# Kernel optimization log

Measured on AMD Instinct MI355X. Metric: run time of the kernel, lower is better.

Reference implementation:

```python
import jax, jax.numpy as jnp
import numpy as np


def rotary_pos_emb(x):
    # x: [b, h, l, k]; interleaved rotary embedding (pairs are (0,1),(2,3),...)
    dim = x.shape[-1]
    seq = x.shape[-2]
    ts = jnp.arange(0, dim, 2, dtype=jnp.float32)
    inv_freqs = 10000.0 ** (-ts / dim)                      # [dim/2]
    grid = jnp.arange(seq, dtype=jnp.float32)[:, None] * inv_freqs[None, :]  # [l, dim/2]
    sin_embs = jnp.repeat(jnp.sin(grid), 2, axis=-1)[None]  # [1, l, dim] (interleaved repeat)
    cos_embs = jnp.repeat(jnp.cos(grid), 2, axis=-1)[None]
    x1, x2 = x[..., ::2], x[..., 1::2]
    xs = jnp.stack([-x2, x1], axis=-1).reshape(x.shape)     # interleave (-x2, x1)
    return x * cos_embs + xs * sin_embs


def setup_inputs() -> dict:
    key = jax.random.key(0)
    ks = jax.random.split(key, 5)
    b, l, d = 2, 2048, 1024
    scale = 1.0 / np.sqrt(d)
    return {
        "x": jax.random.normal(ks[0], (b, l, d), dtype=jnp.float32),
        "Wq": jax.random.normal(ks[1], (d, d), dtype=jnp.float32) * scale,
        "Wk": jax.random.normal(ks[2], (d, d), dtype=jnp.float32) * scale,
        "Wv": jax.random.normal(ks[3], (d, d), dtype=jnp.float32) * scale,
        "Wo": jax.random.normal(ks[4], (d, d), dtype=jnp.float32) * scale,
        "is_training": 0,
    }


def reference(x, Wq, Wk, Wv, Wo, is_training):
    n_heads = 16
    b, l, d = x.shape
    k_size = d // n_heads
    # NOTE: module scales q by 1/sqrt(model_size), not 1/sqrt(key_size)
    q = (x @ Wq) / jnp.sqrt(jnp.float32(d))
    q = q.reshape(b, l, n_heads, k_size).transpose(0, 2, 1, 3)  # b h l k
    k = (x @ Wk).reshape(b, l, n_heads, k_size).transpose(0, 2, 1, 3)
    v = (x @ Wv).reshape(b, l, n_heads, k_size).transpose(0, 2, 1, 3)
    q = rotary_pos_emb(q)
    k = rotary_pos_emb(k)
    logits = jnp.einsum('bhik,bhjk->bhij', q, k)  # no mask, no dropout (eval)
    a = jax.nn.softmax(logits, axis=-1)
    y = jnp.einsum('bhij,bhjv->bhiv', a, v)
    y = y.transpose(0, 2, 1, 3).reshape(b, l, d)  # b l (h v)
    return y @ Wo
```

## Files before the change

### kernel.cpp

```cpp
#include <hip/hip_runtime.h>
#include <stdint.h>

typedef unsigned short u16;
using short8 = __attribute__((ext_vector_type(8))) short;
using f32x4  = __attribute__((ext_vector_type(4))) float;

typedef __attribute__((address_space(1))) unsigned int gu32;
typedef __attribute__((address_space(3))) unsigned int lu32;

__device__ __forceinline__ void gl2lds16(const u16* g, u16* lds_wave_base) {
    __builtin_amdgcn_global_load_lds(
        (gu32*)(uintptr_t)(const void*)g,
        (lu32*)(uint32_t)(uintptr_t)(void*)lds_wave_base,
        16, 0, 0);
}

__device__ inline float bf2f(u16 u) {
    union { unsigned int i; float f; } v;
    v.i = ((unsigned int)u) << 16;
    return v.f;
}
__device__ inline u16 f2bf(float f) {
    union { float f; unsigned int i; } v;
    v.f = f;
    unsigned int x = v.i;
    return (u16)((x + 0x7fffu + ((x >> 16) & 1u)) >> 16);
}
__device__ inline u16 f2bf_trunc(float f) {
    union { float f; unsigned int i; } v;
    v.f = f;
    return (u16)(v.i >> 16);
}

__global__ __launch_bounds__(256) void cvt_x(const float* __restrict__ x,
                                             u16* __restrict__ xb)
{
    int i = (blockIdx.x * 256 + threadIdx.x) * 4;
    float4 v = *(const float4*)(x + i);
    ushort4 o;
    o.x = f2bf(v.x); o.y = f2bf(v.y); o.z = f2bf(v.z); o.w = f2bf(v.w);
    *(ushort4*)(xb + i) = o;
}

__global__ __launch_bounds__(256) void transpose4_cvt(
    const float* __restrict__ w0, const float* __restrict__ w1,
    const float* __restrict__ w2, const float* __restrict__ w3,
    u16* __restrict__ t0, u16* __restrict__ t1,
    u16* __restrict__ t2, u16* __restrict__ t3)
{
    __shared__ u16 tile[32][33];
    const float* src; u16* dst;
    switch (blockIdx.z) {
        case 0:  src = w0; dst = t0; break;
        case 1:  src = w1; dst = t1; break;
        case 2:  src = w2; dst = t2; break;
        default: src = w3; dst = t3; break;
    }
    int tx = threadIdx.x, ty = threadIdx.y;
    int c0 = blockIdx.x * 32, r0 = blockIdx.y * 32;
    #pragma unroll
    for (int i = 0; i < 4; i++)
        tile[ty + i * 8][tx] = f2bf(src[(size_t)(r0 + ty + i * 8) * 1024 + c0 + tx]);
    __syncthreads();
    #pragma unroll
    for (int i = 0; i < 4; i++)
        dst[(size_t)(c0 + ty + i * 8) * 1024 + r0 + tx] = tile[tx][ty + i * 8];
}

__global__ __launch_bounds__(256) void transpose_v(const u16* __restrict__ Vb,
                                                   u16* __restrict__ VT)
{
    __shared__ u16 t[32][33];
    int bh = blockIdx.z, b = bh >> 4, h = bh & 15;
    int p0 = blockIdx.x * 32, c0 = blockIdx.y * 32;
    int tx = threadIdx.x, ty = threadIdx.y;
    #pragma unroll
    for (int i = 0; i < 4; i++)
        t[ty + i * 8][tx] = Vb[(size_t)(b * 2048 + p0 + ty + i * 8) * 1024 + h * 64 + c0 + tx];
    __syncthreads();
    #pragma unroll
    for (int i = 0; i < 4; i++)
        VT[((size_t)bh * 64 + c0 + ty + i * 8) * 2048 + p0 + tx] = t[tx][ty + i * 8];
}

__global__ __launch_bounds__(256) void gemm_qkv(
    const u16* __restrict__ A, const u16* __restrict__ Bt,
    u16* __restrict__ Qb, u16* __restrict__ Kb, u16* __restrict__ Vb)
{
    __shared__ __align__(16) u16 As[128 * 32];
    __shared__ __align__(16) u16 Bs[128 * 32];

    const int tid  = threadIdx.x;
    const int lane = tid & 63;
    const int wid  = tid >> 6;
    const int quad = lane >> 4;
    const int l15  = lane & 15;
    const int wm   = wid >> 1, wn = wid & 1;

    const int m0 = blockIdx.y * 128;
    const int n0 = blockIdx.x * 128;
    const int mat = n0 >> 10;
    const int ln0 = n0 & 1023;
    u16* C = (mat == 0) ? Qb : (mat == 1 ? Kb : Vb);
    const float scale = (mat == 0) ? 0.03125f : 1.0f;

    f32x4 acc[4][4] = {};

    for (int k0 = 0; k0 < 1024; k0 += 32) {
        #pragma unroll
        for (int it = 0; it < 2; it++) {
            int c   = it * 256 + tid;
            int row = c >> 2;
            int col = ((c & 3) ^ (row & 3)) * 8;
            u16* lbA = &As[(size_t)(it * 256 + wid * 64) * 8];
            u16* lbB = &Bs[(size_t)(it * 256 + wid * 64) * 8];
            gl2lds16(&A [(size_t)(m0 + row) * 1024 + k0 + col], lbA);
            gl2lds16(&Bt[(size_t)(n0 + row) * 1024 + k0 + col], lbB);
        }
        __syncthreads();

        short8 a[4], b[4];
        #pragma unroll
        for (int i = 0; i < 4; i++) {
            int ra = wm * 64 + i * 16 + l15;
            int rb = wn * 64 + i * 16 + l15;
            a[i] = *(const short8*)(&As[ra * 32 + ((quad ^ (ra & 3)) * 8)]);
            b[i] = *(const short8*)(&Bs[rb * 32 + ((quad ^ (rb & 3)) * 8)]);
        }
        #pragma unroll
        for (int i = 0; i < 4; i++)
            #pragma unroll
            for (int j = 0; j < 4; j++)
                acc[i][j] = __builtin_amdgcn_mfma_f32_16x16x32_bf16(a[i], b[j], acc[i][j], 0, 0, 0);
        __syncthreads();
    }

    #pragma unroll
    for (int i = 0; i < 4; i++)
        #pragma unroll
        for (int j = 0; j < 4; j++)
            #pragma unroll
            for (int r = 0; r < 4; r++) {
                int row = m0 + wm * 64 + i * 16 + quad * 4 + r;
                int col = ln0 + wn * 64 + j * 16 + l15;
                C[(size_t)row * 1024 + col] = f2bf(acc[i][j][r] * scale);
            }
}

__global__ __launch_bounds__(256) void gemm_out(
    const u16* __restrict__ A, const u16* __restrict__ Bt, float* __restrict__ C)
{
    __shared__ __align__(16) u16 As[128 * 32];
    __shared__ __align__(16) u16 Bs[128 * 32];

    const int tid  = threadIdx.x;
    const int lane = tid & 63;
    const int wid  = tid >> 6;
    const int quad = lane >> 4;
    const int l15  = lane & 15;
    const int wm   = wid >> 1, wn = wid & 1;

    const int m0 = blockIdx.y * 128;
    const int n0 = blockIdx.x * 128;

    f32x4 acc[4][4] = {};

    for (int k0 = 0; k0 < 1024; k0 += 32) {
        #pragma unroll
        for (int it = 0; it < 2; it++) {
            int c   = it * 256 + tid;
            int row = c >> 2;
            int col = ((c & 3) ^ (row & 3)) * 8;
            u16* lbA = &As[(size_t)(it * 256 + wid * 64) * 8];
            u16* lbB = &Bs[(size_t)(it * 256 + wid * 64) * 8];
            gl2lds16(&A [(size_t)(m0 + row) * 1024 + k0 + col], lbA);
            gl2lds16(&Bt[(size_t)(n0 + row) * 1024 + k0 + col], lbB);
        }
        __syncthreads();

        short8 a[4], b[4];
        #pragma unroll
        for (int i = 0; i < 4; i++) {
            int ra = wm * 64 + i * 16 + l15;
            int rb = wn * 64 + i * 16 + l15;
            a[i] = *(const short8*)(&As[ra * 32 + ((quad ^ (ra & 3)) * 8)]);
            b[i] = *(const short8*)(&Bs[rb * 32 + ((quad ^ (rb & 3)) * 8)]);
        }
        #pragma unroll
        for (int i = 0; i < 4; i++)
            #pragma unroll
            for (int j = 0; j < 4; j++)
                acc[i][j] = __builtin_amdgcn_mfma_f32_16x16x32_bf16(a[i], b[j], acc[i][j], 0, 0, 0);
        __syncthreads();
    }

    #pragma unroll
    for (int i = 0; i < 4; i++)
        #pragma unroll
        for (int j = 0; j < 4; j++)
            #pragma unroll
            for (int r = 0; r < 4; r++) {
                int row = m0 + wm * 64 + i * 16 + quad * 4 + r;
                int col = n0 + wn * 64 + j * 16 + l15;
                C[(size_t)row * 1024 + col] = acc[i][j][r];
            }
}

__global__ __launch_bounds__(256) void rope_k(u16* __restrict__ Q, u16* __restrict__ Kb)
{
    u16* buf = (blockIdx.y == 0) ? Q : Kb;
    int idx = blockIdx.x * 256 + threadIdx.x;
    int row = idx >> 9;
    int p   = idx & 511;
    int pos = row & 2047;
    int i   = p & 31;

    const float ln10000_over_32 = 0.2878231366f;
    float inv = __expf(-(float)i * ln10000_over_32);
    float ang = (float)pos * inv;
    float s, c;
    __sincosf(ang, &s, &c);

    size_t base = (size_t)row * 1024 + (size_t)p * 2;
    float x0 = bf2f(buf[base]);
    float x1 = bf2f(buf[base + 1]);
    buf[base]     = f2bf(x0 * c - x1 * s);
    buf[base + 1] = f2bf(x1 * c + x0 * s);
}

__global__ __launch_bounds__(256) void attn(
    const u16* __restrict__ Q, const u16* __restrict__ Kb,
    const u16* __restrict__ VT, u16* __restrict__ Y)
{
    __shared__ __align__(16) u16 Ks [64 * 64];
    __shared__ __align__(16) u16 VTs[64 * 64];
    __shared__ __align__(16) u16 Ps [4][16 * 72];

    const int tid  = threadIdx.x;
    const int lane = tid & 63, wid = tid >> 6;
    const int quad = lane >> 4, l15 = lane & 15;

    const int bh = blockIdx.x;
    const int qt = blockIdx.y;
    const int bb = bh >> 4, h = bh & 15;

    const size_t base = ((size_t)bb * 2048) * 1024 + (size_t)h * 64;

    short8 qf[2];
    {
        size_t qrow = (size_t)qt * 64 + wid * 16 + l15;
        const u16* qp = Q + base + qrow * 1024;
        qf[0] = *(const short8*)(qp + quad * 8);
        qf[1] = *(const short8*)(qp + 32 + quad * 8);
    }

    f32x4 o[4] = {};
    float l_r[4] = {0.f, 0.f, 0.f, 0.f};

    for (int j0 = 0; j0 < 2048; j0 += 64) {
        __syncthreads();
        #pragma unroll
        for (int it = 0; it < 2; it++) {
            int c   = it * 256 + tid;
            int r   = c >> 3;
            int col = ((c & 7) ^ (r & 7)) * 8;
            u16* lbK = &Ks [(size_t)(it * 256 + wid * 64) * 8];
            u16* lbV = &VTs[(size_t)(it * 256 + wid * 64) * 8];
            gl2lds16(&Kb[base + (size_t)(j0 + r) * 1024 + col], lbK);
            gl2lds16(&VT[((size_t)bh * 64 + r) * 2048 + j0 + col], lbV);
        }
        __syncthreads();

        f32x4 s[4];
        #pragma unroll
        for (int nt = 0; nt < 4; nt++) {
            int R = nt * 16 + l15;
            short8 k0 = *(const short8*)(&Ks[R * 64 + (( quad      ^ (R & 7)) * 8)]);
            short8 k1 = *(const short8*)(&Ks[R * 64 + (((quad + 4) ^ (R & 7)) * 8)]);
            f32x4 z = {};
            z = __builtin_amdgcn_mfma_f32_16x16x32_bf16(qf[0], k0, z, 0, 0, 0);
            z = __builtin_amdgcn_mfma_f32_16x16x32_bf16(qf[1], k1, z, 0, 0, 0);
            s[nt] = z;
        }

        #pragma unroll
        for (int nt = 0; nt < 4; nt++)
            #pragma unroll
            for (int r = 0; r < 4; r++) {
                float p = __expf(s[nt][r]);
                l_r[r] += p;
                Ps[wid][(quad * 4 + r) * 72 + nt * 16 + l15] = f2bf_trunc(p);
            }

        asm volatile("s_waitcnt lgkmcnt(0)" ::: "memory");

        short8 pa0 = *(const short8*)(&Ps[wid][l15 * 72 + quad * 8]);
        short8 pa1 = *(const short8*)(&Ps[wid][l15 * 72 + 32 + quad * 8]);
        #pragma unroll
        for (int nt = 0; nt < 4; nt++) {
            int R = nt * 16 + l15;
            short8 vb0 = *(const short8*)(&VTs[R * 64 + (( quad      ^ (R & 7)) * 8)]);
            short8 vb1 = *(const short8*)(&VTs[R * 64 + (((quad + 4) ^ (R & 7)) * 8)]);
            o[nt] = __builtin_amdgcn_mfma_f32_16x16x32_bf16(pa0, vb0, o[nt], 0, 0, 0);
            o[nt] = __builtin_amdgcn_mfma_f32_16x16x32_bf16(pa1, vb1, o[nt], 0, 0, 0);
        }
    }

    #pragma unroll
    for (int r = 0; r < 4; r++) {
        l_r[r] += __shfl_xor(l_r[r], 1);
        l_r[r] += __shfl_xor(l_r[r], 2);
        l_r[r] += __shfl_xor(l_r[r], 4);
        l_r[r] += __shfl_xor(l_r[r], 8);
        l_r[r] = 1.0f / l_r[r];
    }

    size_t qrow0 = (size_t)qt * 64 + wid * 16;
    #pragma unroll
    for (int nt = 0; nt < 4; nt++)
        #pragma unroll
        for (int r = 0; r < 4; r++) {
            size_t row = qrow0 + quad * 4 + r;
            Y[base + row * 1024 + nt * 16 + l15] = f2bf(o[nt][r] * l_r[r]);
        }
}

extern "C" void kernel_launch(void* const* d_in, const int* in_sizes, int n_in,
                              void* d_out, int out_size, void* d_ws, size_t ws_size,
                              hipStream_t stream)
{
    const float* x  = (const float*)d_in[0];
    const float* Wq = (const float*)d_in[1];
    const float* Wk = (const float*)d_in[2];
    const float* Wv = (const float*)d_in[3];
    const float* Wo = (const float*)d_in[4];
    float* out = (float*)d_out;

    char* ws = (char*)d_ws;
    u16* xb     = (u16*)(ws + (0ull  << 20));
    u16* WqkvT  = (u16*)(ws + (8ull  << 20));
    u16* WoT    = (u16*)(ws + (14ull << 20));
    u16* Qb     = (u16*)(ws + (16ull << 20));
    u16* Kb     = (u16*)(ws + (24ull << 20));
    u16* Vb     = (u16*)(ws + (32ull << 20));
    u16* VTb    = (u16*)(ws + (40ull << 20));
    u16* Yb     = (u16*)(ws + (48ull << 20));

    cvt_x<<<4096, 256, 0, stream>>>(x, xb);
    transpose4_cvt<<<dim3(32, 32, 4), dim3(32, 8), 0, stream>>>(
        Wq, Wk, Wv, Wo,
        WqkvT, WqkvT + (1024ull * 1024), WqkvT + (2048ull * 1024), WoT);
    gemm_qkv<<<dim3(24, 32), 256, 0, stream>>>(xb, WqkvT, Qb, Kb, Vb);
    rope_k<<<dim3(8192, 2), 256, 0, stream>>>(Qb, Kb);
    transpose_v<<<dim3(64, 2, 32), dim3(32, 8), 0, stream>>>(Vb, VTb);
    attn<<<dim3(32, 32), 256, 0, stream>>>(Qb, Kb, VTb, Yb);
    gemm_out<<<dim3(8, 32), 256, 0, stream>>>(Yb, WoT, out);
}
```

Before: 219.3 us.

## Fuse RoPE into QKV GEMM epilogue and widen attention KV tile

Removes the standalone RoPE kernel and applies the rotary rotation in the QKV GEMM epilogue, taking the pair partner from the neighbouring lane via a shuffle. The Q scale now folds in log2(e) so attention can use exp2 directly. The attention loop processes 128 keys per iteration instead of 64, with larger K/V LDS tiles and an XOR-swizzled P buffer in place of padding, which halves the barrier count. The cost is more epilogue work and larger LDS use, which may lower attention occupancy.

Result: faster. 210.1 us (-4.2%).

```diff
diff --git a/kernel.cpp b/kernel.cpp
--- a/kernel.cpp
+++ b/kernel.cpp
@@ -102,7 +102,6 @@
     const int mat = n0 >> 10;
     const int ln0 = n0 & 1023;
     u16* C = (mat == 0) ? Qb : (mat == 1 ? Kb : Vb);
-    const float scale = (mat == 0) ? 0.03125f : 1.0f;
 
     f32x4 acc[4][4] = {};
 
@@ -135,6 +134,11 @@
         __syncthreads();
     }
 
+    const float scale = (mat == 0) ? (0.03125f * 1.44269504f) : 1.0f;
+    const float l2_10000_over_32 = 0.41524101186f;
+    const bool do_rope = (mat < 2);
+    const int odd = l15 & 1;
+
     #pragma unroll
     for (int i = 0; i < 4; i++)
         #pragma unroll
@@ -143,7 +147,21 @@
             for (int r = 0; r < 4; r++) {
                 int row = m0 + wm * 64 + i * 16 + quad * 4 + r;
                 int col = ln0 + wn * 64 + j * 16 + l15;
-                C[(size_t)row * 1024 + col] = f2bf(acc[i][j][r] * scale);
+                float v = acc[i][j][r] * scale;
+                float outv;
+                if (do_rope) {
+                    float vp = __shfl_xor(v, 1);
+                    int pi   = (col & 63) >> 1;
+                    int pos  = row & 2047;
+                    float ang = (float)pos *
+                        __builtin_amdgcn_exp2f(-(float)pi * l2_10000_over_32);
+                    float sn, cs;
+                    __sincosf(ang, &sn, &cs);
+                    outv = odd ? (v * cs + vp * sn) : (v * cs - vp * sn);
+                } else {
+                    outv = v;
+                }
+                C[(size_t)row * 1024 + col] = f2bf(outv);
             }
 }
 
@@ -206,35 +224,13 @@
             }
 }
 
-__global__ __launch_bounds__(256) void rope_k(u16* __restrict__ Q, u16* __restrict__ Kb)
-{
-    u16* buf = (blockIdx.y == 0) ? Q : Kb;
-    int idx = blockIdx.x * 256 + threadIdx.x;
-    int row = idx >> 9;
-    int p   = idx & 511;
-    int pos = row & 2047;
-    int i   = p & 31;
-
-    const float ln10000_over_32 = 0.2878231366f;
-    float inv = __expf(-(float)i * ln10000_over_32);
-    float ang = (float)pos * inv;
-    float s, c;
-    __sincosf(ang, &s, &c);
-
-    size_t base = (size_t)row * 1024 + (size_t)p * 2;
-    float x0 = bf2f(buf[base]);
-    float x1 = bf2f(buf[base + 1]);
-    buf[base]     = f2bf(x0 * c - x1 * s);
-    buf[base + 1] = f2bf(x1 * c + x0 * s);
-}
-
 __global__ __launch_bounds__(256) void attn(
     const u16* __restrict__ Q, const u16* __restrict__ Kb,
     const u16* __restrict__ VT, u16* __restrict__ Y)
 {
-    __shared__ __align__(16) u16 Ks [64 * 64];
-    __shared__ __align__(16) u16 VTs[64 * 64];
-    __shared__ __align__(16) u16 Ps [4][16 * 72];
+    __shared__ __align__(16) u16 Ks [128 * 64];
+    __shared__ __align__(16) u16 VTs[64 * 128];
+    __shared__ __align__(16) u16 Ps [4][16 * 64];
 
     const int tid  = threadIdx.x;
     const int lane = tid & 63, wid = tid >> 6;
@@ -257,23 +253,23 @@
     f32x4 o[4] = {};
     float l_r[4] = {0.f, 0.f, 0.f, 0.f};
 
-    for (int j0 = 0; j0 < 2048; j0 += 64) {
-        __syncthreads();
-        #pragma unroll
-        for (int it = 0; it < 2; it++) {
-            int c   = it * 256 + tid;
-            int r   = c >> 3;
-            int col = ((c & 7) ^ (r & 7)) * 8;
+    for (int j0 = 0; j0 < 2048; j0 += 128) {
+        __syncthreads();
+        #pragma unroll
+        for (int it = 0; it < 4; it++) {
+            int c = it * 256 + tid;
+            int rk = c >> 3, ck = ((c & 7)  ^ (rk & 7))  * 8;
+            int rv = c >> 4, cv = ((c & 15) ^ (rv & 15)) * 8;
             u16* lbK = &Ks [(size_t)(it * 256 + wid * 64) * 8];
             u16* lbV = &VTs[(size_t)(it * 256 + wid * 64) * 8];
-            gl2lds16(&Kb[base + (size_t)(j0 + r) * 1024 + col], lbK);
-            gl2lds16(&VT[((size_t)bh * 64 + r) * 2048 + j0 + col], lbV);
-        }
-        __syncthreads();
-
-        f32x4 s[4];
-        #pragma unroll
-        for (int nt = 0; nt < 4; nt++) {
+            gl2lds16(&Kb[base + (size_t)(j0 + rk) * 1024 + ck], lbK);
+            gl2lds16(&VT[((size_t)bh * 64 + rv) * 2048 + j0 + cv], lbV);
+        }
+        __syncthreads();
+
+        f32x4 s[8];
+        #pragma unroll
+        for (int nt = 0; nt < 8; nt++) {
             int R = nt * 16 + l15;
             short8 k0 = *(const short8*)(&Ks[R * 64 + (( quad      ^ (R & 7)) * 8)]);
             short8 k1 = *(const short8*)(&Ks[R * 64 + (((quad + 4) ^ (R & 7)) * 8)]);
@@ -284,25 +280,33 @@
         }
 
         #pragma unroll
-        for (int nt = 0; nt < 4; nt++)
-            #pragma unroll
-            for (int r = 0; r < 4; r++) {
-                float p = __expf(s[nt][r]);
-                l_r[r] += p;
-                Ps[wid][(quad * 4 + r) * 72 + nt * 16 + l15] = f2bf_trunc(p);
+        for (int hh = 0; hh < 2; hh++) {
+            #pragma unroll
+            for (int n4 = 0; n4 < 4; n4++) {
+                int nt = hh * 4 + n4;
+                #pragma unroll
+                for (int r = 0; r < 4; r++) {
+                    float p = __builtin_amdgcn_exp2f(s[nt][r]);
+                    l_r[r] += p;
+                    int m = quad * 4 + r;
+                    int col = n4 * 16 + l15;
+                    Ps[wid][m * 64 + (((col >> 3) ^ (m & 7)) * 8) + (col & 7)]
+                        = f2bf_trunc(p);
+                }
             }
-
-        asm volatile("s_waitcnt lgkmcnt(0)" ::: "memory");
-
-        short8 pa0 = *(const short8*)(&Ps[wid][l15 * 72 + quad * 8]);
-        short8 pa1 = *(const short8*)(&Ps[wid][l15 * 72 + 32 + quad * 8]);
-        #pragma unroll
-        for (int nt = 0; nt < 4; nt++) {
-            int R = nt * 16 + l15;
-            short8 vb0 = *(const short8*)(&VTs[R * 64 + (( quad      ^ (R & 7)) * 8)]);
-            short8 vb1 = *(const short8*)(&VTs[R * 64 + (((quad + 4) ^ (R & 7)) * 8)]);
-            o[nt] = __builtin_amdgcn_mfma_f32_16x16x32_bf16(pa0, vb0, o[nt], 0, 0, 0);
-            o[nt] = __builtin_amdgcn_mfma_f32_16x16x32_bf16(pa1, vb1, o[nt], 0, 0, 0);
+            asm volatile("s_waitcnt lgkmcnt(0)" ::: "memory");
+
+            short8 pa0 = *(const short8*)(&Ps[wid][l15 * 64 + (( quad      ^ (l15 & 7)) * 8)]);
+            short8 pa1 = *(const short8*)(&Ps[wid][l15 * 64 + (((quad + 4) ^ (l15 & 7)) * 8)]);
+            #pragma unroll
+            for (int nt = 0; nt < 4; nt++) {
+                int R = nt * 16 + l15;
+                short8 vb0 = *(const short8*)(&VTs[R * 128 + (((hh * 8 + quad)     ^ (R & 15)) * 8)]);
+                short8 vb1 = *(const short8*)(&VTs[R * 128 + (((hh * 8 + quad + 4) ^ (R & 15)) * 8)]);
+                o[nt] = __builtin_amdgcn_mfma_f32_16x16x32_bf16(pa0, vb0, o[nt], 0, 0, 0);
+                o[nt] = __builtin_amdgcn_mfma_f32_16x16x32_bf16(pa1, vb1, o[nt], 0, 0, 0);
+            }
+            asm volatile("" ::: "memory");
         }
     }
 
@@ -351,7 +355,6 @@
         Wq, Wk, Wv, Wo,
         WqkvT, WqkvT + (1024ull * 1024), WqkvT + (2048ull * 1024), WoT);
     gemm_qkv<<<dim3(24, 32), 256, 0, stream>>>(xb, WqkvT, Qb, Kb, Vb);
-    rope_k<<<dim3(8192, 2), 256, 0, stream>>>(Qb, Kb);
     transpose_v<<<dim3(64, 2, 32), dim3(32, 8), 0, stream>>>(Vb, VTb);
     attn<<<dim3(32, 32), 256, 0, stream>>>(Qb, Kb, VTb, Yb);
     gemm_out<<<dim3(8, 32), 256, 0, stream>>>(Yb, WoT, out);
```
